# Kernel optimization log

Measured on AMD Instinct MI355X. Metric: run time of the kernel, lower is better.

Reference implementation:

```python
import jax, jax.numpy as jnp
import numpy as np

N_NODES = 100000


def _gat_conv(x, edge_index, W, att_src, att_dst, bias, concat):
    """PyG-style GATConv (eval mode, self-loops already in edge_index).
    x: [N, F_in], W: [F_in, H*C], att_*: [H, C], bias: [H*C] or [C].
    """
    N = x.shape[0]
    H, C = att_src.shape
    xl = (x @ W).reshape(N, H, C)                      # [N, H, C]
    a_src = jnp.einsum('nhc,hc->nh', xl, att_src)      # [N, H]
    a_dst = jnp.einsum('nhc,hc->nh', xl, att_dst)      # [N, H]
    src, dst = edge_index[0], edge_index[1]
    e = jax.nn.leaky_relu(a_src[src] + a_dst[dst], negative_slope=0.2)  # [E, H]
    # segment softmax over incoming edges per destination node
    e_max = jax.ops.segment_max(e, dst, num_segments=N)                 # [N, H]
    e_exp = jnp.exp(e - e_max[dst])                                     # [E, H]
    denom = jax.ops.segment_sum(e_exp, dst, num_segments=N)             # [N, H]
    alpha = e_exp / (denom[dst] + 1e-16)                                # [E, H]
    msg = xl[src] * alpha[:, :, None]                                   # [E, H, C]
    out = jax.ops.segment_sum(msg, dst, num_segments=N)                 # [N, H, C]
    out = out.reshape(N, H * C) if concat else out.mean(axis=1)
    return out + bias


def setup_inputs() -> dict:
    key = jax.random.key(0)
    ks = jax.random.split(key, 12)
    in_dim, hidden, heads, out_dim = 128, 16, 8, 64
    E = 1600000
    x = jax.random.normal(ks[0], (N_NODES, in_dim), dtype=jnp.float32)
    edge_index = jax.random.randint(ks[1], (2, E), 0, N_NODES, dtype=jnp.int32)
    s1 = 1.0 / np.sqrt(in_dim)
    s2 = 1.0 / np.sqrt(hidden * heads)
    return {
        'x': x,
        'edge_index': edge_index,
        'W1': jax.random.normal(ks[2], (in_dim, heads * hidden), dtype=jnp.float32) * s1,
        'att_src1': jax.random.normal(ks[3], (heads, hidden), dtype=jnp.float32) * 0.1,
        'att_dst1': jax.random.normal(ks[4], (heads, hidden), dtype=jnp.float32) * 0.1,
        'b1': jnp.zeros((heads * hidden,), dtype=jnp.float32),
        'W2': jax.random.normal(ks[5], (heads * hidden, out_dim), dtype=jnp.float32) * s2,
        'att_src2': jax.random.normal(ks[6], (1, out_dim), dtype=jnp.float32) * 0.1,
        'att_dst2': jax.random.normal(ks[7], (1, out_dim), dtype=jnp.float32) * 0.1,
        'b2': jnp.zeros((out_dim,), dtype=jnp.float32),
    }


def reference(x, edge_index, W1, att_src1, att_dst1, b1, W2, att_src2, att_dst2, b2):
    N = x.shape[0]
    # PyG GATConv default add_self_loops=True
    loops = jnp.tile(jnp.arange(N, dtype=edge_index.dtype), (2, 1))
    ei = jnp.concatenate([edge_index, loops], axis=1)
    h = _gat_conv(x, ei, W1, att_src1, att_dst1, b1, concat=True)
    h = jax.nn.elu(h)
    # dropout is identity in eval mode
    out = _gat_conv(h, ei, W2, att_src2, att_dst2, b2, concat=False)
    return out
```

## Files before the change

### kernel.cpp

```cpp
#include <hip/hip_runtime.h>
#include <cmath>

typedef _Float16 half8 __attribute__((ext_vector_type(8)));
typedef float f32x4 __attribute__((ext_vector_type(4)));

#define CAP 48
#define RTPB 2048
#define SEGCAP 408

__device__ __forceinline__ float elu1(float v) {
    return v > 0.f ? v : (__expf(v) - 1.f);
}

__global__ __launch_bounds__(256) void k_route(
    const int* __restrict__ src, const int* __restrict__ dst, int E, int RB, int npc,
    int* __restrict__ routed, int* __restrict__ pbc,
    const float* __restrict__ W2, _Float16* __restrict__ W2h)
{
    __shared__ int cnt8[8];
    int t = threadIdx.x;
    int b = (int)blockIdx.x;

    if (b == RB) {
        for (int i = t; i < 128 * 64; i += 256) {
            int k = i >> 6, n = i & 63;
            W2h[n * 128 + k] = (_Float16)W2[i];
        }
        return;
    }

    if (t < 8) cnt8[t] = 0;

    size_t e0 = (size_t)b * RTPB + t;
    int sv[8], cv[8], ov[8];
#pragma unroll
    for (int k = 0; k < 8; k++) {
        size_t e = e0 + (size_t)k * 256;
        int s = 0, d = 0, c = -1;
        if (e < (size_t)E) {
            s = src[e]; d = dst[e];
            c = (d >= npc) + (d >= 2 * npc) + (d >= 3 * npc) + (d >= 4 * npc)
              + (d >= 5 * npc) + (d >= 6 * npc) + (d >= 7 * npc);
        }
        sv[k] = s; cv[k] = c; ov[k] = d - c * npc;
    }
    __syncthreads();
    int pos[8];
#pragma unroll
    for (int k = 0; k < 8; k++)
        pos[k] = cv[k] >= 0 ? atomicAdd(&cnt8[cv[k]], 1) : 0;
    __syncthreads();
#pragma unroll
    for (int k = 0; k < 8; k++) {
        int c = cv[k];
        if (c >= 0 && pos[k] < SEGCAP)
            routed[((size_t)c * RB + b) * SEGCAP + pos[k]] = (sv[k] << 14) | ov[k];
    }
    if (t < 8) pbc[t * RB + b] = cnt8[t] < SEGCAP ? cnt8[t] : SEGCAP;
}

__global__ __launch_bounds__(256) void k_build(
    int* __restrict__ cnt, int* __restrict__ sorted,
    const int* __restrict__ routed, const int* __restrict__ pbc,
    int RB, int npc, int SGRP, int GGRP, int R, int GB,
    const float* __restrict__ x, const float* __restrict__ W,
    const float* __restrict__ att_s, const float* __restrict__ att_d,
    _Float16* __restrict__ xlh, _Float16* __restrict__ a_s, float* __restrict__ a_d, int N)
{
    __shared__ _Float16 Wt[128 * 72];
    int t = threadIdx.x;
    int bid = (int)blockIdx.x;
    int grp = bid >> 3;

    bool isSc;
    int sgrp, gx;
    if (R >= 2) {
        int q = grp / R, rem = grp - q * R;
        isSc = (rem == R - 1) && (q < SGRP);
        int sb = q < SGRP ? q : SGRP;
        sgrp = q;
        gx = (grp - sb) * 8 + (bid & 7);
    } else {
        isSc = grp < SGRP;
        sgrp = grp;
        gx = (grp - SGRP) * 8 + (bid & 7);
    }

    if (isSc) {
        int c = bid & 7;
        int lo = c * npc;
        int hi = lo + npc; if (hi > N) hi = N;
        for (int i = sgrp * 256 + t; i < hi - lo; i += SGRP * 256) {
            int d = lo + i;
            int pos = atomicAdd(&cnt[d], 1);
            if (pos < CAP) sorted[(size_t)d * CAP + pos] = d;
        }
        for (int b = sgrp; b < RB; b += SGRP) {
            int m = pbc[c * RB + b];
            const int* seg = routed + ((size_t)c * RB + b) * SEGCAP;
            for (int i = t; i < m; i += 256) {
                int u = seg[i];
                int d = lo + (u & 16383);
                int s = (int)((unsigned)u >> 14);
                int pos = atomicAdd(&cnt[d], 1);
                if (pos < CAP) sorted[(size_t)d * CAP + pos] = s;
            }
        }
        return;
    }

    int bx = gx;
    if (bx >= GB) return;
    int wave = t >> 6, lane = t & 63;
    int cl = lane & 15, quad = lane >> 4;
    int arow = bx * 64 + wave * 16 + cl;
    int rr = arow < N ? arow : N - 1;

    half8 af[4];
#pragma unroll
    for (int ks = 0; ks < 4; ks++) {
        const float4* p = (const float4*)(x + (size_t)rr * 128 + ks * 32 + quad * 8);
        float4 A = p[0], B = p[1];
        af[ks][0] = (_Float16)A.x; af[ks][1] = (_Float16)A.y;
        af[ks][2] = (_Float16)A.z; af[ks][3] = (_Float16)A.w;
        af[ks][4] = (_Float16)B.x; af[ks][5] = (_Float16)B.y;
        af[ks][6] = (_Float16)B.z; af[ks][7] = (_Float16)B.w;
    }

    f32x4 acc[8];
#pragma unroll
    for (int nt = 0; nt < 8; nt++) acc[nt] = (f32x4){0.f, 0.f, 0.f, 0.f};

#pragma unroll
    for (int h = 0; h < 2; h++) {
        if (h) __syncthreads();
        for (int i = t; i < 128 * 64; i += 256) {
            int k0 = i >> 7, n = i & 127;
            Wt[n * 72 + (k0 ^ (((n >> 3) & 7) << 3))] =
                (_Float16)W[(size_t)(h * 64 + k0) * 128 + n];
        }
        __syncthreads();
#pragma unroll
        for (int nt = 0; nt < 8; nt++) {
            int n = nt * 16 + cl;
            int swz = ((n >> 3) & 7) << 3;
#pragma unroll
            for (int ks2 = 0; ks2 < 2; ks2++) {
                half8 bf = *(const half8*)&Wt[n * 72 + ((ks2 * 32 + quad * 8) ^ swz)];
                acc[nt] = __builtin_amdgcn_mfma_f32_16x16x32_f16(
                    af[h * 2 + ks2], bf, acc[nt], 0, 0, 0);
            }
        }
    }

    float asl[8], adl[8];
#pragma unroll
    for (int nt = 0; nt < 8; nt++) {
        asl[nt] = att_s[nt * 16 + cl];
        adl[nt] = att_d[nt * 16 + cl];
    }

    int rbase = bx * 64 + wave * 16 + quad * 4;
#pragma unroll
    for (int r = 0; r < 4; r++) {
        int orow = rbase + r;
        bool ok = orow < N;
#pragma unroll
        for (int nt = 0; nt < 8; nt++) {
            float v = acc[nt][r];
            if (ok) xlh[(size_t)orow * 128 + nt * 16 + cl] = (_Float16)v;
        }
#pragma unroll
        for (int nt = 0; nt < 8; nt++) {
            float ps = acc[nt][r] * asl[nt];
            float pd = acc[nt][r] * adl[nt];
            ps += __shfl_xor(ps, 1); ps += __shfl_xor(ps, 2);
            ps += __shfl_xor(ps, 4); ps += __shfl_xor(ps, 8);
            pd += __shfl_xor(pd, 1); pd += __shfl_xor(pd, 2);
            pd += __shfl_xor(pd, 4); pd += __shfl_xor(pd, 8);
            if (ok && cl == 0) {
                a_s[(size_t)orow * 8 + nt] = (_Float16)ps;
                a_d[(size_t)orow * 8 + nt] = pd;
            }
        }
    }
}

__global__ __launch_bounds__(256) void k_agg1_gemm2(
    const int* __restrict__ cnt, const int* __restrict__ ss,
    const _Float16* __restrict__ as, const float* __restrict__ ad,
    const _Float16* __restrict__ xlh, const float* __restrict__ b1,
    const _Float16* __restrict__ W2h,
    const float* __restrict__ att_s2, const float* __restrict__ att_d2,
    _Float16* __restrict__ xl2h, float* __restrict__ a_s2, float* __restrict__ a_d2, int N)
{
    __shared__ _Float16 Ht[32 * 136];
    __shared__ float asb[2][32], adb[2][32];

    int t = threadIdx.x;

    int ln = t >> 3;
    int g = blockIdx.x * 32 + ln;
    int lane8 = t & 7;
    int c = lane8 * 16;
    {
        int gg = g < N ? g : N - 1;
        int deg = cnt[gg]; deg = deg < CAP ? deg : CAP;
        int start = gg * CAP, end = start + deg;
        float adv = ad[(size_t)gg * 8 + lane8];

        float l = 0.f;
        float acc[16];
#pragma unroll
        for (int j = 0; j < 16; j++) acc[j] = 0.f;

        int i = start;
        for (; i + 4 <= end; i += 4) {
            int s0 = ss[i], s1 = ss[i + 1], s2 = ss[i + 2], s3 = ss[i + 3];
            float a0 = (float)as[(size_t)s0 * 8 + lane8];
            float a1 = (float)as[(size_t)s1 * 8 + lane8];
            float a2 = (float)as[(size_t)s2 * 8 + lane8];
            float a3 = (float)as[(size_t)s3 * 8 + lane8];
            const _Float16* p0 = xlh + (size_t)s0 * 128 + c;
            const _Float16* p1 = xlh + (size_t)s1 * 128 + c;
            const _Float16* p2 = xlh + (size_t)s2 * 128 + c;
            const _Float16* p3 = xlh + (size_t)s3 * 128 + c;
            half8 x0a = *(const half8*)p0, x0b = *(const half8*)(p0 + 8);
            half8 x1a = *(const half8*)p1, x1b = *(const half8*)(p1 + 8);
            half8 x2a = *(const half8*)p2, x2b = *(const half8*)(p2 + 8);
            half8 x3a = *(const half8*)p3, x3b = *(const half8*)(p3 + 8);
            float v0 = a0 + adv; v0 = v0 > 0.f ? v0 : 0.2f * v0;
            float v1 = a1 + adv; v1 = v1 > 0.f ? v1 : 0.2f * v1;
            float v2 = a2 + adv; v2 = v2 > 0.f ? v2 : 0.2f * v2;
            float v3 = a3 + adv; v3 = v3 > 0.f ? v3 : 0.2f * v3;
            float w0 = __expf(v0), w1 = __expf(v1);
            float w2 = __expf(v2), w3 = __expf(v3);
            l += (w0 + w1) + (w2 + w3);
#pragma unroll
            for (int j = 0; j < 8; j++) {
                acc[j]     += ((float)x0a[j] * w0 + (float)x1a[j] * w1)
                            + ((float)x2a[j] * w2 + (float)x3a[j] * w3);
                acc[j + 8] += ((float)x0b[j] * w0 + (float)x1b[j] * w1)
                            + ((float)x2b[j] * w2 + (float)x3b[j] * w3);
            }
        }
        for (; i < end; i++) {
            int s0 = ss[i];
            float v0 = (float)as[(size_t)s0 * 8 + lane8] + adv;
            v0 = v0 > 0.f ? v0 : 0.2f * v0;
            float w0 = __expf(v0);
            l += w0;
            const _Float16* p0 = xlh + (size_t)s0 * 128 + c;
            half8 x0a = *(const half8*)p0, x0b = *(const half8*)(p0 + 8);
#pragma unroll
            for (int j = 0; j < 8; j++) {
                acc[j]     += (float)x0a[j] * w0;
                acc[j + 8] += (float)x0b[j] * w0;
            }
        }
        float inv = 1.f / (l + 1e-16f);
        float4 bq[4];
        bq[0] = *(const float4*)(b1 + c);
        bq[1] = *(const float4*)(b1 + c + 4);
        bq[2] = *(const float4*)(b1 + c + 8);
        bq[3] = *(const float4*)(b1 + c + 12);
        const float* bb = (const float*)bq;
        half8 o0, o1;
#pragma unroll
        for (int j = 0; j < 8; j++) {
            o0[j] = (_Float16)elu1(acc[j] * inv + bb[j]);
            o1[j] = (_Float16)elu1(acc[j + 8] * inv + bb[j + 8]);
        }
        *(half8*)&Ht[ln * 136 + c] = o0;
        *(half8*)&Ht[ln * 136 + c + 8] = o1;
    }
    __syncthreads();

    int wave = t >> 6, lane = t & 63;
    int cl = lane & 15, quad = lane >> 4;
    int rt = wave >> 1;
    int half = wave & 1;

    half8 af[4];
#pragma unroll
    for (int ks = 0; ks < 4; ks++)
        af[ks] = *(const half8*)&Ht[(rt * 16 + cl) * 136 + ks * 32 + quad * 8];

    f32x4 acc2[2];
    acc2[0] = (f32x4){0.f, 0.f, 0.f, 0.f};
    acc2[1] = (f32x4){0.f, 0.f, 0.f, 0.f};
    float asl[2], adl[2];
#pragma unroll
    for (int ntl = 0; ntl < 2; ntl++) {
        int n = (half * 2 + ntl) * 16 + cl;
        asl[ntl] = att_s2[n];
        adl[ntl] = att_d2[n];
#pragma unroll
        for (int ks = 0; ks < 4; ks++) {
            half8 bf = *(const half8*)&W2h[n * 128 + ks * 32 + quad * 8];
            acc2[ntl] = __builtin_amdgcn_mfma_f32_16x16x32_f16(af[ks], bf, acc2[ntl], 0, 0, 0);
        }
    }

#pragma unroll
    for (int r = 0; r < 4; r++) {
        int lrow = rt * 16 + quad * 4 + r;
        int orow = blockIdx.x * 32 + lrow;
        bool ok = orow < N;
        float ps = 0.f, pd = 0.f;
#pragma unroll
        for (int ntl = 0; ntl < 2; ntl++) {
            float v = acc2[ntl][r];
            if (ok) xl2h[(size_t)orow * 64 + (half * 2 + ntl) * 16 + cl] = (_Float16)v;
            ps += v * asl[ntl];
            pd += v * adl[ntl];
        }
        ps += __shfl_xor(ps, 1); ps += __shfl_xor(ps, 2);
        ps += __shfl_xor(ps, 4); ps += __shfl_xor(ps, 8);
        pd += __shfl_xor(pd, 1); pd += __shfl_xor(pd, 2);
        pd += __shfl_xor(pd, 4); pd += __shfl_xor(pd, 8);
        if (cl == 0) { asb[half][lrow] = ps; adb[half][lrow] = pd; }
    }
    __syncthreads();
    if (t < 32) {
        int orow = blockIdx.x * 32 + t;
        if (orow < N) {
            a_s2[orow] = asb[0][t] + asb[1][t];
            a_d2[orow] = adb[0][t] + adb[1][t];
        }
    }
}

__global__ __launch_bounds__(256) void k_agg2(
    const int* __restrict__ cnt, const int* __restrict__ ss,
    const float* __restrict__ as, const float* __restrict__ ad,
    const _Float16* __restrict__ xlh, const float* __restrict__ b2,
    float* __restrict__ out, int N)
{
    int t = threadIdx.x;
    int g = (blockIdx.x * 256 + t) >> 3;
    if (g >= N) return;
    int lane = t & 7;
    int c = lane * 8;
    int deg = cnt[g]; deg = deg < CAP ? deg : CAP;
    int start = g * CAP, end = start + deg;
    float adv = ad[g];

    float l = 0.f;
    float acc[8];
#pragma unroll
    for (int j = 0; j < 8; j++) acc[j] = 0.f;

    int i = start;
    for (; i + 8 <= end; i += 8) {
        int sv[8];
#pragma unroll
        for (int u = 0; u < 8; u++) sv[u] = ss[i + u];
        float av[8];
#pragma unroll
        for (int u = 0; u < 8; u++) av[u] = as[sv[u]];
        half8 xv[8];
#pragma unroll
        for (int u = 0; u < 8; u++)
            xv[u] = *(const half8*)(xlh + (size_t)sv[u] * 64 + c);
        float wv[8];
#pragma unroll
        for (int u = 0; u < 8; u++) {
            float v = av[u] + adv;
            v = v > 0.f ? v : 0.2f * v;
            wv[u] = __expf(v);
        }
        l += ((wv[0] + wv[1]) + (wv[2] + wv[3])) + ((wv[4] + wv[5]) + (wv[6] + wv[7]));
#pragma unroll
        for (int j = 0; j < 8; j++) {
            float s01 = (float)xv[0][j] * wv[0] + (float)xv[1][j] * wv[1];
            float s23 = (float)xv[2][j] * wv[2] + (float)xv[3][j] * wv[3];
            float s45 = (float)xv[4][j] * wv[4] + (float)xv[5][j] * wv[5];
            float s67 = (float)xv[6][j] * wv[6] + (float)xv[7][j] * wv[7];
            acc[j] += (s01 + s23) + (s45 + s67);
        }
    }
    for (; i + 4 <= end; i += 4) {
        int s0 = ss[i], s1 = ss[i + 1], s2 = ss[i + 2], s3 = ss[i + 3];
        float a0 = as[s0], a1 = as[s1], a2 = as[s2], a3 = as[s3];
        half8 x0 = *(const half8*)(xlh + (size_t)s0 * 64 + c);
        half8 x1 = *(const half8*)(xlh + (size_t)s1 * 64 + c);
        half8 x2 = *(const half8*)(xlh + (size_t)s2 * 64 + c);
        half8 x3 = *(const half8*)(xlh + (size_t)s3 * 64 + c);
        float v0 = a0 + adv; v0 = v0 > 0.f ? v0 : 0.2f * v0;
        float v1 = a1 + adv; v1 = v1 > 0.f ? v1 : 0.2f * v1;
        float v2 = a2 + adv; v2 = v2 > 0.f ? v2 : 0.2f * v2;
        float v3 = a3 + adv; v3 = v3 > 0.f ? v3 : 0.2f * v3;
        float w0 = __expf(v0), w1 = __expf(v1), w2 = __expf(v2), w3 = __expf(v3);
        l += (w0 + w1) + (w2 + w3);
#pragma unroll
        for (int j = 0; j < 8; j++)
            acc[j] += ((float)x0[j] * w0 + (float)x1[j] * w1)
                    + ((float)x2[j] * w2 + (float)x3[j] * w3);
    }
    for (; i < end; i++) {
        int s0 = ss[i];
        float v0 = as[s0] + adv;
        v0 = v0 > 0.f ? v0 : 0.2f * v0;
        float w0 = __expf(v0);
        l += w0;
        half8 x0 = *(const half8*)(xlh + (size_t)s0 * 64 + c);
#pragma unroll
        for (int j = 0; j < 8; j++) acc[j] += (float)x0[j] * w0;
    }
    float inv = 1.f / (l + 1e-16f);
    float4 b0 = *(const float4*)(b2 + c);
    float4 b4 = *(const float4*)(b2 + c + 4);
    float bb[8] = {b0.x, b0.y, b0.z, b0.w, b4.x, b4.y, b4.z, b4.w};
    float4 o0, o1;
    o0.x = acc[0] * inv + bb[0];
    o0.y = acc[1] * inv + bb[1];
    o0.z = acc[2] * inv + bb[2];
    o0.w = acc[3] * inv + bb[3];
    o1.x = acc[4] * inv + bb[4];
    o1.y = acc[5] * inv + bb[5];
    o1.z = acc[6] * inv + bb[6];
    o1.w = acc[7] * inv + bb[7];
    *(float4*)(out + (size_t)g * 64 + c) = o0;
    *(float4*)(out + (size_t)g * 64 + c + 4) = o1;
}

extern "C" void kernel_launch(void* const* d_in, const int* in_sizes, int n_in,
                              void* d_out, int out_size, void* d_ws, size_t ws_size,
                              hipStream_t stream) {
    const float* x   = (const float*)d_in[0];
    const int*   ei  = (const int*)  d_in[1];
    const float* W1  = (const float*)d_in[2];
    const float* as1 = (const float*)d_in[3];
    const float* ad1 = (const float*)d_in[4];
    const float* b1  = (const float*)d_in[5];
    const float* W2  = (const float*)d_in[6];
    const float* as2 = (const float*)d_in[7];
    const float* ad2 = (const float*)d_in[8];
    const float* b2  = (const float*)d_in[9];

    const int N = in_sizes[0] / 128;
    const int E = in_sizes[1] / 2;
    const int npc = (N + 7) / 8;
    if (N > 131072) return;
    const int RB = (E + RTPB - 1) / RTPB;
    const int SGRP = (E / 8 + npc + 2047) / 2048;
    const int GB = (N + 63) / 64;
    const int GGRP = (GB + 7) / 8;
    const int Tg = SGRP + GGRP;
    int R = SGRP > 0 ? Tg / SGRP : 0;
    const int* src = ei;
    const int* dst = ei + E;

    float* ws    = (float*)d_ws;
    _Float16* xl1h = (_Float16*)ws;
    _Float16* as1h = (_Float16*)(ws + (size_t)N * 64);
    float* ad1v  = ws + (size_t)N * 68;
    _Float16* xl2h = (_Float16*)(ad1v + (size_t)N * 8);
    float* as2v  = ad1v + (size_t)N * 8 + (size_t)N * 32;
    float* ad2v  = as2v + (size_t)N;
    int*   cnt   = (int*)(ad2v + (size_t)N);
    int*   sorted= cnt + (size_t)N;
    int*   pbc   = sorted + (size_t)N * CAP;
    int*   routed= pbc + (size_t)RB * 8;
    _Float16* W2h = (_Float16*)(routed + (size_t)RB * 8 * SEGCAP);
    float* out   = (float*)d_out;

    size_t need = ((size_t)N * (111 + CAP) + (size_t)RB * 8 * (1 + SEGCAP) + 4096) * 4;
    if (ws_size < need) return;

    hipMemsetAsync(cnt, 0, (size_t)N * 4, stream);

    k_route<<<RB + 1, 256, 0, stream>>>(src, dst, E, RB, npc, routed, pbc, W2, W2h);

    k_build<<<Tg * 8, 256, 0, stream>>>(
        cnt, sorted, routed, pbc, RB, npc, SGRP, GGRP, R, GB,
        x, W1, as1, ad1, xl1h, as1h, ad1v, N);

    k_agg1_gemm2<<<(N + 31) / 32, 256, 0, stream>>>(
        cnt, sorted, as1h, ad1v, xl1h, b1, W2h, as2, ad2, xl2h, as2v, ad2v, N);

    k_agg2 <<<(int)(((size_t)N * 8 + 255) / 256), 256, 0, stream>>>(
        cnt, sorted, as2v, ad2v, xl2h, b2, out, N);
}
```

Before: 327.2 us.

## Route edges into 2048-node chunks and count in shared memory

Edge routing now splits destinations into 64 fixed 2048-node chunks, not 8 large ones. Each chunk is then bucketed by a single build block that counts with shared-memory atomics and writes the final counts itself. This removes the global count memset and the global atomics. W1 is also converted once to transposed fp16 in the route kernel, so GEMM blocks read it straight from global memory instead of restaging it through LDS. Workspace is reorganized so the routed buffer aliases the later layer-2 buffers. The trade-off is that the scatter phase now runs on only about 49 blocks, each thread walking many segments serially, which can limit parallelism.

```diff
diff --git a/kernel.cpp b/kernel.cpp
--- a/kernel.cpp
+++ b/kernel.cpp
@@ -6,22 +6,27 @@
 
 #define CAP 48
 #define RTPB 2048
-#define SEGCAP 408
+#define SEGC 96
 
 __device__ __forceinline__ float elu1(float v) {
     return v > 0.f ? v : (__expf(v) - 1.f);
 }
 
 __global__ __launch_bounds__(256) void k_route(
-    const int* __restrict__ src, const int* __restrict__ dst, int E, int RB, int npc,
+    const int* __restrict__ src, const int* __restrict__ dst, int E, int RB, int NC,
     int* __restrict__ routed, int* __restrict__ pbc,
+    const float* __restrict__ W1, _Float16* __restrict__ W1h,
     const float* __restrict__ W2, _Float16* __restrict__ W2h)
 {
-    __shared__ int cnt8[8];
+    __shared__ int cntc[64];
     int t = threadIdx.x;
     int b = (int)blockIdx.x;
 
     if (b == RB) {
+        for (int i = t; i < 128 * 128; i += 256) {
+            int k = i >> 7, n = i & 127;
+            W1h[n * 128 + k] = (_Float16)W1[i];
+        }
         for (int i = t; i < 128 * 64; i += 256) {
             int k = i >> 6, n = i & 63;
             W2h[n * 128 + k] = (_Float16)W2[i];
@@ -29,7 +34,7 @@
         return;
     }
 
-    if (t < 8) cnt8[t] = 0;
+    if (t < NC) cntc[t] = 0;
 
     size_t e0 = (size_t)b * RTPB + t;
     int sv[8], cv[8], ov[8];
@@ -39,77 +44,67 @@
         int s = 0, d = 0, c = -1;
         if (e < (size_t)E) {
             s = src[e]; d = dst[e];
-            c = (d >= npc) + (d >= 2 * npc) + (d >= 3 * npc) + (d >= 4 * npc)
-              + (d >= 5 * npc) + (d >= 6 * npc) + (d >= 7 * npc);
-        }
-        sv[k] = s; cv[k] = c; ov[k] = d - c * npc;
+            c = d >> 11;
+        }
+        sv[k] = s; cv[k] = c; ov[k] = d & 2047;
     }
     __syncthreads();
     int pos[8];
 #pragma unroll
     for (int k = 0; k < 8; k++)
-        pos[k] = cv[k] >= 0 ? atomicAdd(&cnt8[cv[k]], 1) : 0;
+        pos[k] = cv[k] >= 0 ? atomicAdd(&cntc[cv[k]], 1) : 0;
     __syncthreads();
 #pragma unroll
     for (int k = 0; k < 8; k++) {
         int c = cv[k];
-        if (c >= 0 && pos[k] < SEGCAP)
-            routed[((size_t)c * RB + b) * SEGCAP + pos[k]] = (sv[k] << 14) | ov[k];
-    }
-    if (t < 8) pbc[t * RB + b] = cnt8[t] < SEGCAP ? cnt8[t] : SEGCAP;
+        if (c >= 0 && pos[k] < SEGC)
+            routed[((size_t)c * RB + b) * SEGC + pos[k]] = (sv[k] << 11) | ov[k];
+    }
+    if (t < NC) pbc[t * RB + b] = cntc[t] < SEGC ? cntc[t] : SEGC;
 }
 
 __global__ __launch_bounds__(256) void k_build(
     int* __restrict__ cnt, int* __restrict__ sorted,
     const int* __restrict__ routed, const int* __restrict__ pbc,
-    int RB, int npc, int SGRP, int GGRP, int R, int GB,
-    const float* __restrict__ x, const float* __restrict__ W,
+    int RB, int NC, int GB,
+    const float* __restrict__ x, const _Float16* __restrict__ W1h,
     const float* __restrict__ att_s, const float* __restrict__ att_d,
     _Float16* __restrict__ xlh, _Float16* __restrict__ a_s, float* __restrict__ a_d, int N)
 {
-    __shared__ _Float16 Wt[128 * 72];
+    __shared__ int lcnt[2048];
     int t = threadIdx.x;
     int bid = (int)blockIdx.x;
-    int grp = bid >> 3;
-
-    bool isSc;
-    int sgrp, gx;
-    if (R >= 2) {
-        int q = grp / R, rem = grp - q * R;
-        isSc = (rem == R - 1) && (q < SGRP);
-        int sb = q < SGRP ? q : SGRP;
-        sgrp = q;
-        gx = (grp - sb) * 8 + (bid & 7);
-    } else {
-        isSc = grp < SGRP;
-        sgrp = grp;
-        gx = (grp - SGRP) * 8 + (bid & 7);
-    }
-
-    if (isSc) {
-        int c = bid & 7;
-        int lo = c * npc;
-        int hi = lo + npc; if (hi > N) hi = N;
-        for (int i = sgrp * 256 + t; i < hi - lo; i += SGRP * 256) {
-            int d = lo + i;
-            int pos = atomicAdd(&cnt[d], 1);
-            if (pos < CAP) sorted[(size_t)d * CAP + pos] = d;
-        }
-        for (int b = sgrp; b < RB; b += SGRP) {
-            int m = pbc[c * RB + b];
-            const int* seg = routed + ((size_t)c * RB + b) * SEGCAP;
-            for (int i = t; i < m; i += 256) {
+
+    if (bid < NC) {
+        int lo = bid << 11;
+        int hi = lo + 2048; if (hi > N) hi = N;
+        int range = hi - lo;
+        for (int i = t; i < range; i += 256) lcnt[i] = 0;
+        __syncthreads();
+        for (int i = t; i < range; i += 256) {
+            int pos = atomicAdd(&lcnt[i], 1);
+            if (pos < CAP) sorted[(size_t)(lo + i) * CAP + pos] = lo + i;
+        }
+        for (int b = t; b < RB; b += 256) {
+            int m = pbc[bid * RB + b];
+            const int* seg = routed + ((size_t)bid * RB + b) * SEGC;
+            for (int i = 0; i < m; i++) {
                 int u = seg[i];
-                int d = lo + (u & 16383);
-                int s = (int)((unsigned)u >> 14);
-                int pos = atomicAdd(&cnt[d], 1);
-                if (pos < CAP) sorted[(size_t)d * CAP + pos] = s;
+                int doff = u & 2047;
+                int s = (int)((unsigned)u >> 11);
+                int pos = atomicAdd(&lcnt[doff], 1);
+                if (pos < CAP) sorted[(size_t)(lo + doff) * CAP + pos] = s;
             }
         }
+        __syncthreads();
+        for (int i = t; i < range; i += 256) {
+            int cv = lcnt[i];
+            cnt[lo + i] = cv < CAP ? cv : CAP;
+        }
         return;
     }
 
-    int bx = gx;
+    int bx = bid - NC;
     if (bx >= GB) return;
     int wave = t >> 6, lane = t & 63;
     int cl = lane & 15, quad = lane >> 4;
@@ -133,20 +128,12 @@
 
 #pragma unroll
     for (int h = 0; h < 2; h++) {
-        if (h) __syncthreads();
-        for (int i = t; i < 128 * 64; i += 256) {
-            int k0 = i >> 7, n = i & 127;
-            Wt[n * 72 + (k0 ^ (((n >> 3) & 7) << 3))] =
-                (_Float16)W[(size_t)(h * 64 + k0) * 128 + n];
-        }
-        __syncthreads();
 #pragma unroll
         for (int nt = 0; nt < 8; nt++) {
             int n = nt * 16 + cl;
-            int swz = ((n >> 3) & 7) << 3;
 #pragma unroll
             for (int ks2 = 0; ks2 < 2; ks2++) {
-                half8 bf = *(const half8*)&Wt[n * 72 + ((ks2 * 32 + quad * 8) ^ swz)];
+                half8 bf = *(const half8*)&W1h[n * 128 + h * 64 + ks2 * 32 + quad * 8];
                 acc[nt] = __builtin_amdgcn_mfma_f32_16x16x32_f16(
                     af[h * 2 + ks2], bf, acc[nt], 0, 0, 0);
             }
@@ -441,14 +428,10 @@
 
     const int N = in_sizes[0] / 128;
     const int E = in_sizes[1] / 2;
-    const int npc = (N + 7) / 8;
     if (N > 131072) return;
     const int RB = (E + RTPB - 1) / RTPB;
-    const int SGRP = (E / 8 + npc + 2047) / 2048;
+    const int NC = (N + 2047) >> 11;
     const int GB = (N + 63) / 64;
-    const int GGRP = (GB + 7) / 8;
-    const int Tg = SGRP + GGRP;
-    int R = SGRP > 0 ? Tg / SGRP : 0;
     const int* src = ei;
     const int* dst = ei + E;
 
@@ -456,26 +439,27 @@
     _Float16* xl1h = (_Float16*)ws;
     _Float16* as1h = (_Float16*)(ws + (size_t)N * 64);
     float* ad1v  = ws + (size_t)N * 68;
-    _Float16* xl2h = (_Float16*)(ad1v + (size_t)N * 8);
-    float* as2v  = ad1v + (size_t)N * 8 + (size_t)N * 32;
-    float* ad2v  = as2v + (size_t)N;
-    int*   cnt   = (int*)(ad2v + (size_t)N);
-    int*   sorted= cnt + (size_t)N;
+    int*   cnt   = (int*)(ws + (size_t)N * 76);
+    int*   sorted= cnt + N;
     int*   pbc   = sorted + (size_t)N * CAP;
-    int*   routed= pbc + (size_t)RB * 8;
-    _Float16* W2h = (_Float16*)(routed + (size_t)RB * 8 * SEGCAP);
+    _Float16* W1h = (_Float16*)(pbc + (size_t)RB * 64);
+    _Float16* W2h = W1h + 16384;
+    float* scratch = (float*)(W2h + 8192);
+    int*   routed = (int*)scratch;
+    _Float16* xl2h = (_Float16*)scratch;
+    float* as2v  = scratch + (size_t)N * 32;
+    float* ad2v  = as2v + N;
     float* out   = (float*)d_out;
 
-    size_t need = ((size_t)N * (111 + CAP) + (size_t)RB * 8 * (1 + SEGCAP) + 4096) * 4;
+    size_t scrA = (size_t)RB * 64 * SEGC, scrB = (size_t)N * 34;
+    size_t need = ((size_t)N * 125 + (size_t)RB * 64 + 12288 + (scrA > scrB ? scrA : scrB)) * 4;
     if (ws_size < need) return;
 
-    hipMemsetAsync(cnt, 0, (size_t)N * 4, stream);
-
-    k_route<<<RB + 1, 256, 0, stream>>>(src, dst, E, RB, npc, routed, pbc, W2, W2h);
-
-    k_build<<<Tg * 8, 256, 0, stream>>>(
-        cnt, sorted, routed, pbc, RB, npc, SGRP, GGRP, R, GB,
-        x, W1, as1, ad1, xl1h, as1h, ad1v, N);
+    k_route<<<RB + 1, 256, 0, stream>>>(src, dst, E, RB, NC, routed, pbc, W1, W1h, W2, W2h);
+
+    k_build<<<NC + GB, 256, 0, stream>>>(
+        cnt, sorted, routed, pbc, RB, NC, GB,
+        x, W1h, as1, ad1, xl1h, as1h, ad1v, N);
 
     k_agg1_gemm2<<<(N + 31) / 32, 256, 0, stream>>>(
         cnt, sorted, as1h, ad1v, xl1h, b1, W2h, as2, ad2, xl2h, as2v, ad2v, N);
```

Result: slower. 361.3 us (+10.4%).
